# Optimization experiments

Measured on AMD Instinct MI355X. Metric: run time of the kernel, lower is better.

## Reference

```python
import jax, jax.numpy as jnp
import numpy as np


def setup_inputs() -> dict:
    key = jax.random.key(0)
    k1, k2, k3, k4 = jax.random.split(key, 4)
    n, C, t, h, w = 1, 256, 8, 64, 64
    heads = 8
    S = t + h + w - 2  # 134 axial positions per query
    attention = jax.random.normal(k1, (n, heads * S, t, h, w), dtype=jnp.float32)
    value = jax.random.normal(k2, (n, C, t, h, w), dtype=jnp.float32)
    conv_w = jax.random.normal(k3, (C, C), dtype=jnp.float32) / np.float32(np.sqrt(C))
    conv_b = jax.random.normal(k4, (C,), dtype=jnp.float32)
    return {"attention": attention, "value": value, "conv_w": conv_w,
            "conv_b": conv_b, "num_heads": heads}


def _grid_attn_map(A, V):
    """Criss-cross axial attention aggregation.
    A: [b, t+h+w-2, t, h, w] per-query weights over the t-axis (t entries,
       self included), h-axis (h-1 entries, self excluded) and w-axis
       (w-1 entries, self excluded).
    V: [b, c, t, h, w]. Returns [b, c, t, h, w].
    """
    b, c, t, h, w = V.shape
    A_t = A[:, :t]                  # [b, t, t, h, w]
    A_h = A[:, t:t + h - 1]         # [b, h-1, t, h, w]
    A_w = A[:, t + h - 1:]          # [b, w-1, t, h, w]

    # t-axis (self included): sum over key frame s
    out = jnp.einsum('bsthw,bcshw->bcthw', A_t, V)

    # h-axis (self excluded): channel j addresses key row p = j + (j >= q).
    # Build dense [h] channel axis with a zero at p == q via a padded gather.
    zpad = jnp.zeros((b, 1, t, h, w), A.dtype)
    A_h_pad = jnp.concatenate([A_h, zpad], axis=1)  # channel h-1 is zero
    p = jnp.arange(h)[:, None]
    q = jnp.arange(h)[None, :]
    inv_h = jnp.where(p < q, p, jnp.where(p == q, h - 1, p - 1))  # [h(p), h(q)]
    A_h_full = jnp.take_along_axis(A_h_pad, inv_h[None, :, None, :, None], axis=1)  # [b,p,t,q,w]
    out = out + jnp.einsum('bptqw,bctpw->bctqw', A_h_full, V)

    # w-axis (self excluded), same trick along w
    A_w_pad = jnp.concatenate([A_w, zpad], axis=1)  # channel w-1 is zero (h==w here OK; recompute pad generally)
    pw = jnp.arange(w)[:, None]
    qw = jnp.arange(w)[None, :]
    inv_w = jnp.where(pw < qw, pw, jnp.where(pw == qw, w - 1, pw - 1))  # [w(p), w(q)]
    A_w_full = jnp.take_along_axis(A_w_pad, inv_w[None, :, None, None, :], axis=1)  # [b,p,t,h,q]
    out = out + jnp.einsum('bpthq,bcthp->bcthq', A_w_full, V)
    return out


def reference(attention, value, conv_w, conv_b, num_heads):
    n, C, t, h, w = value.shape
    S = t + h + w - 2
    # 1x1x1 Conv3d == per-position channel matmul
    pv = jnp.einsum('ncthw,oc->nothw', value, conv_w) + conv_b[None, :, None, None, None]
    pv = pv.reshape(n * num_heads, C // num_heads, t, h, w)
    A = attention.reshape(n * num_heads, S, t, h, w)
    out = _grid_attn_map(A, pv)
    return out.reshape(n, num_heads, C // num_heads, t, h, w)
```

## Files before the change

### kernel.cpp

```cpp
#include <hip/hip_runtime.h>

#define SS   134
#define HWP  4096
#define THW  32768

typedef float f32x4 __attribute__((ext_vector_type(4)));
typedef short bf16x8 __attribute__((ext_vector_type(8)));
typedef short bf16x4 __attribute__((ext_vector_type(4)));

__device__ __forceinline__ unsigned short f2bf(float f) {
  unsigned int u = __float_as_uint(f);
  u += 0x7fff + ((u >> 16) & 1);
  return (unsigned short)(u >> 16);
}

__global__ __launch_bounds__(256) void conv1x1_v2(
    const float* __restrict__ V, const float* __restrict__ W,
    const float* __restrict__ bias, float* __restrict__ PV) {
  __shared__ unsigned short sW[256 * 40];
  __shared__ unsigned short sV[32 * 40];
  const int tid = threadIdx.x;
  const int x0 = blockIdx.x * 32;
  const int lane = tid & 63;
  const int wv = tid >> 6;
  const int m = lane & 15;
  const int q = lane >> 4;

  f32x4 acc[4][2];
#pragma unroll
  for (int i = 0; i < 4; ++i)
#pragma unroll
    for (int j = 0; j < 2; ++j)
      acc[i][j] = (f32x4){0.f, 0.f, 0.f, 0.f};

  for (int k0 = 0; k0 < 256; k0 += 32) {
#pragma unroll 2
    for (int r = 0; r < 8; ++r) {
      const int f = r * 256 + tid;
      const int o = f >> 3;
      const int c4 = (f & 7) * 4;
      const float4 w4 = *(const float4*)&W[o * 256 + k0 + c4];
      bf16x4 b;
      b.x = (short)f2bf(w4.x);
      b.y = (short)f2bf(w4.y);
      b.z = (short)f2bf(w4.z);
      b.w = (short)f2bf(w4.w);
      *(bf16x4*)&sW[o * 40 + c4] = b;
    }
    {
      const int c = tid >> 3;
      const int x4 = (tid & 7) * 4;
      const float4 v4 = *(const float4*)&V[(size_t)(k0 + c) * THW + x0 + x4];
      sV[(x4 + 0) * 40 + c] = f2bf(v4.x);
      sV[(x4 + 1) * 40 + c] = f2bf(v4.y);
      sV[(x4 + 2) * 40 + c] = f2bf(v4.z);
      sV[(x4 + 3) * 40 + c] = f2bf(v4.w);
    }
    __syncthreads();
    bf16x8 fa[4], fb[2];
#pragma unroll
    for (int i = 0; i < 4; ++i)
      fa[i] = *(const bf16x8*)&sW[(wv * 64 + i * 16 + m) * 40 + q * 8];
#pragma unroll
    for (int j = 0; j < 2; ++j)
      fb[j] = *(const bf16x8*)&sV[(j * 16 + m) * 40 + q * 8];
#pragma unroll
    for (int i = 0; i < 4; ++i)
#pragma unroll
      for (int j = 0; j < 2; ++j)
        acc[i][j] = __builtin_amdgcn_mfma_f32_16x16x32_bf16(fa[i], fb[j], acc[i][j], 0, 0, 0);
    __syncthreads();
  }

#pragma unroll
  for (int i = 0; i < 4; ++i) {
#pragma unroll
    for (int r = 0; r < 4; ++r) {
      const int o = wv * 64 + i * 16 + q * 4 + r;
      const float b = bias[o];
#pragma unroll
      for (int j = 0; j < 2; ++j)
        PV[(size_t)o * THW + x0 + j * 16 + m] = acc[i][j][r] + b;
    }
  }
}

__global__ __launch_bounds__(256) void attn_th(
    const float* __restrict__ A, const float* __restrict__ PV,
    float* __restrict__ O) {
  const int b = blockIdx.x;
  const int wb = b & 7;
  const int tq = (b >> 3) & 7;
  const int hd = b >> 6;
  const int tid = threadIdx.x;
  const int w4 = (tid & 1) * 4;
  const int q16 = (tid >> 1) & 15;
  const int cg = tid >> 5;

  __shared__ float slab[32 * 64 * 8];

  const float* __restrict__ Ab = A + (size_t)hd * SS * THW + (size_t)tq * HWP;
  const size_t pvh = (size_t)hd * 32 * THW;

#pragma unroll 4
  for (int i = 0; i < 16; ++i) {
    const int fid = tid + i * 256;
    const int ws = (fid & 1) * 4;
    const int p = (fid >> 1) & 63;
    const int c = fid >> 7;
    *(f32x4*)&slab[(c * 64 + p) * 8 + ws] =
        *(const f32x4*)&PV[pvh + (size_t)c * THW + (size_t)tq * HWP + p * 64 + wb * 8 + ws];
  }
  __syncthreads();

  f32x4 acc[4][4];
#pragma unroll
  for (int i = 0; i < 4; ++i)
#pragma unroll
    for (int j = 0; j < 4; ++j)
      acc[i][j] = (f32x4){0.f, 0.f, 0.f, 0.f};

  for (int s = 0; s < 8; ++s) {
#pragma unroll
    for (int qq = 0; qq < 4; ++qq) {
      const int q = qq * 16 + q16;
      const f32x4 a = *(const f32x4*)&Ab[(size_t)s * THW + q * 64 + wb * 8 + w4];
#pragma unroll
      for (int ci = 0; ci < 4; ++ci) {
        const int c = cg + ci * 8;
        const f32x4 v =
            *(const f32x4*)&PV[pvh + (size_t)c * THW + (size_t)s * HWP + q * 64 + wb * 8 + w4];
        acc[qq][ci] += a * v;
      }
    }
  }

  const float* __restrict__ Ah = Ab + (size_t)8 * THW + wb * 8 + w4;
#pragma unroll 2
  for (int p = 0; p < 64; ++p) {
    f32x4 av[4];
#pragma unroll
    for (int qq = 0; qq < 4; ++qq) {
      const int q = qq * 16 + q16;
      const int row = p - (q < p ? 1 : 0);
      f32x4 a = *(const f32x4*)&Ah[(size_t)row * THW + q * 64];
      if (q == p) a = (f32x4){0.f, 0.f, 0.f, 0.f};
      av[qq] = a;
    }
    f32x4 vv[4];
#pragma unroll
    for (int ci = 0; ci < 4; ++ci)
      vv[ci] = *(const f32x4*)&slab[((cg + ci * 8) * 64 + p) * 8 + w4];
#pragma unroll
    for (int qq = 0; qq < 4; ++qq)
#pragma unroll
      for (int ci = 0; ci < 4; ++ci)
        acc[qq][ci] += av[qq] * vv[ci];
  }

#pragma unroll
  for (int qq = 0; qq < 4; ++qq) {
    const int q = qq * 16 + q16;
#pragma unroll
    for (int ci = 0; ci < 4; ++ci) {
      const int c = cg + ci * 8;
      *(f32x4*)&O[pvh + (size_t)c * THW + (size_t)tq * HWP + q * 64 + wb * 8 + w4] =
          acc[qq][ci];
    }
  }
}

__global__ __launch_bounds__(256) void attn_w(
    const float* __restrict__ A, const float* __restrict__ PV,
    float* __restrict__ O) {
  const int b = blockIdx.x;
  const int hb = b & 15;
  const int tq = (b >> 4) & 7;
  const int hd = b >> 7;
  const int tid = threadIdx.x;
  const int wq = tid & 63;
  const int cg = tid >> 6;
  const int h0 = hb * 4;

  __shared__ float slab[32 * 64 * 4];

  const float* __restrict__ Ab = A + (size_t)hd * SS * THW + (size_t)tq * HWP;
  const size_t pvh = (size_t)hd * 32 * THW;

#pragma unroll 4
  for (int i = 0; i < 8; ++i) {
    const int fid = tid + i * 256;
    const int w4s = (fid & 15) * 4;
    const int h = (fid >> 4) & 3;
    const int c = fid >> 6;
    const f32x4 v =
        *(const f32x4*)&PV[pvh + (size_t)c * THW + (size_t)tq * HWP + (h0 + h) * 64 + w4s];
    slab[(c * 64 + w4s + 0) * 4 + h] = v.x;
    slab[(c * 64 + w4s + 1) * 4 + h] = v.y;
    slab[(c * 64 + w4s + 2) * 4 + h] = v.z;
    slab[(c * 64 + w4s + 3) * 4 + h] = v.w;
  }

  f32x4 racc[8];
#pragma unroll
  for (int ci = 0; ci < 8; ++ci) {
    const int c = cg + ci * 4;
    f32x4 r;
#pragma unroll
    for (int hh = 0; hh < 4; ++hh)
      r[hh] = O[pvh + (size_t)c * THW + (size_t)tq * HWP + (h0 + hh) * 64 + wq];
    racc[ci] = r;
  }
  __syncthreads();

#pragma unroll 2
  for (int p = 0; p < 64; ++p) {
    const int row = 71 + p - (wq <= p ? 1 : 0);
    const float* pa = Ab + (size_t)row * THW + h0 * 64 + wq;
    f32x4 a;
    a.x = pa[0];
    a.y = pa[64];
    a.z = pa[128];
    a.w = pa[192];
    if (p == wq) a = (f32x4){0.f, 0.f, 0.f, 0.f};
#pragma unroll
    for (int ci = 0; ci < 8; ++ci) {
      const f32x4 v = *(const f32x4*)&slab[(cg + ci * 4) * 256 + p * 4];
      racc[ci] += a * v;
    }
  }

#pragma unroll
  for (int ci = 0; ci < 8; ++ci) {
    const int c = cg + ci * 4;
#pragma unroll
    for (int hh = 0; hh < 4; ++hh)
      O[pvh + (size_t)c * THW + (size_t)tq * HWP + (h0 + hh) * 64 + wq] = racc[ci][hh];
  }
}

extern "C" void kernel_launch(void* const* d_in, const int* in_sizes, int n_in,
                              void* d_out, int out_size, void* d_ws, size_t ws_size,
                              hipStream_t stream) {
  const float* A = (const float*)d_in[0];
  const float* V = (const float*)d_in[1];
  const float* W = (const float*)d_in[2];
  const float* bias = (const float*)d_in[3];
  float* out = (float*)d_out;
  float* pv = (float*)d_ws;

  conv1x1_v2<<<dim3(1024), 256, 0, stream>>>(V, W, bias, pv);
  attn_th<<<dim3(512), 256, 0, stream>>>(A, pv, out);
  attn_w<<<dim3(1024), 256, 0, stream>>>(A, pv, out);
}
```

Baseline: 380.8 us.

## Retile attn_th over full w rows with double-buffered PV staging in shared memory

attn_th now uses 256 blocks of 512 threads. Each block covers one head, one frame and 16 query rows across the full 64-wide w axis, instead of an 8-wide w strip. The h-axis PV slab is streamed in chunks of 8 rows through a double-buffered 128KB shared buffer, with the next chunk's global loads prefetched into registers while the current chunk is computed. This gives each wave full 256-byte coalesced rows for the A and PV loads and keeps the large slab from limiting occupancy. The cost is fewer blocks (256), extra barriers per chunk, and 128KB of LDS per block, which allows only one block per CU.

```diff
diff --git a/kernel.cpp b/kernel.cpp
--- a/kernel.cpp
+++ b/kernel.cpp
@@ -85,33 +85,27 @@
   }
 }
 
-__global__ __launch_bounds__(256) void attn_th(
+__global__ __launch_bounds__(512) void attn_th(
     const float* __restrict__ A, const float* __restrict__ PV,
     float* __restrict__ O) {
   const int b = blockIdx.x;
-  const int wb = b & 7;
-  const int tq = (b >> 3) & 7;
-  const int hd = b >> 6;
+  const int hd = b & 7;
+  const int qb = (b >> 3) & 3;
+  const int tq = b >> 5;
   const int tid = threadIdx.x;
-  const int w4 = (tid & 1) * 4;
-  const int q16 = (tid >> 1) & 15;
-  const int cg = tid >> 5;
-
-  __shared__ float slab[32 * 64 * 8];
+  const int lane = tid & 63;
+  const int wv = tid >> 6;
+  const int w4 = (lane & 15) * 4;
+  const int cl = lane >> 4;
+  const int ch = wv & 1;
+  const int qg = wv >> 1;
+  const int q0 = qb * 16 + qg * 4;
+
+  __shared__ float slab[2][8 * 32 * 64];
 
   const float* __restrict__ Ab = A + (size_t)hd * SS * THW + (size_t)tq * HWP;
   const size_t pvh = (size_t)hd * 32 * THW;
-
-#pragma unroll 4
-  for (int i = 0; i < 16; ++i) {
-    const int fid = tid + i * 256;
-    const int ws = (fid & 1) * 4;
-    const int p = (fid >> 1) & 63;
-    const int c = fid >> 7;
-    *(f32x4*)&slab[(c * 64 + p) * 8 + ws] =
-        *(const f32x4*)&PV[pvh + (size_t)c * THW + (size_t)tq * HWP + p * 64 + wb * 8 + ws];
-  }
-  __syncthreads();
+  const float* __restrict__ PVh = PV + pvh;
 
   f32x4 acc[4][4];
 #pragma unroll
@@ -120,52 +114,82 @@
     for (int j = 0; j < 4; ++j)
       acc[i][j] = (f32x4){0.f, 0.f, 0.f, 0.f};
 
+  const int c_s = tid >> 4;
+  const int w4s = (tid & 15) * 4;
+  const float* __restrict__ pvstage =
+      PVh + (size_t)c_s * THW + (size_t)tq * HWP + w4s;
+  const int sbase = c_s * 64 + w4s;
+
+  f32x4 stg[8];
+#pragma unroll
+  for (int r = 0; r < 8; ++r) stg[r] = *(const f32x4*)&pvstage[r * 64];
+
   for (int s = 0; s < 8; ++s) {
 #pragma unroll
-    for (int qq = 0; qq < 4; ++qq) {
-      const int q = qq * 16 + q16;
-      const f32x4 a = *(const f32x4*)&Ab[(size_t)s * THW + q * 64 + wb * 8 + w4];
-#pragma unroll
-      for (int ci = 0; ci < 4; ++ci) {
-        const int c = cg + ci * 8;
+    for (int qi = 0; qi < 4; ++qi) {
+      const int q = q0 + qi;
+      const f32x4 a = *(const f32x4*)&Ab[(size_t)s * THW + q * 64 + w4];
+#pragma unroll
+      for (int g = 0; g < 4; ++g) {
+        const int c = ch * 16 + g * 4 + cl;
         const f32x4 v =
-            *(const f32x4*)&PV[pvh + (size_t)c * THW + (size_t)s * HWP + q * 64 + wb * 8 + w4];
-        acc[qq][ci] += a * v;
+            *(const f32x4*)&PVh[(size_t)c * THW + (size_t)s * HWP + q * 64 + w4];
+        acc[qi][g] += a * v;
       }
     }
   }
 
-  const float* __restrict__ Ah = Ab + (size_t)8 * THW + wb * 8 + w4;
-#pragma unroll 2
-  for (int p = 0; p < 64; ++p) {
-    f32x4 av[4];
-#pragma unroll
-    for (int qq = 0; qq < 4; ++qq) {
-      const int q = qq * 16 + q16;
-      const int row = p - (q < p ? 1 : 0);
-      f32x4 a = *(const f32x4*)&Ah[(size_t)row * THW + q * 64];
-      if (q == p) a = (f32x4){0.f, 0.f, 0.f, 0.f};
-      av[qq] = a;
-    }
-    f32x4 vv[4];
-#pragma unroll
-    for (int ci = 0; ci < 4; ++ci)
-      vv[ci] = *(const f32x4*)&slab[((cg + ci * 8) * 64 + p) * 8 + w4];
-#pragma unroll
-    for (int qq = 0; qq < 4; ++qq)
-#pragma unroll
-      for (int ci = 0; ci < 4; ++ci)
-        acc[qq][ci] += av[qq] * vv[ci];
-  }
-
-#pragma unroll
-  for (int qq = 0; qq < 4; ++qq) {
-    const int q = qq * 16 + q16;
-#pragma unroll
-    for (int ci = 0; ci < 4; ++ci) {
-      const int c = cg + ci * 8;
-      *(f32x4*)&O[pvh + (size_t)c * THW + (size_t)tq * HWP + q * 64 + wb * 8 + w4] =
-          acc[qq][ci];
+#pragma unroll
+  for (int r = 0; r < 8; ++r)
+    *(f32x4*)&slab[0][r * 2048 + sbase] = stg[r];
+  __syncthreads();
+
+  for (int ck = 0; ck < 8; ++ck) {
+    const int cur = ck & 1;
+    if (ck < 7) {
+#pragma unroll
+      for (int r = 0; r < 8; ++r)
+        stg[r] = *(const f32x4*)&pvstage[((ck + 1) * 8 + r) * 64];
+    }
+#pragma unroll
+    for (int pp = 0; pp < 8; ++pp) {
+      const int p = ck * 8 + pp;
+      f32x4 a[4];
+#pragma unroll
+      for (int qi = 0; qi < 4; ++qi) {
+        const int q = q0 + qi;
+        const int row = p - (q < p ? 1 : 0);
+        f32x4 av = *(const f32x4*)&Ab[(size_t)(8 + row) * THW + q * 64 + w4];
+        if (q == p) av = (f32x4){0.f, 0.f, 0.f, 0.f};
+        a[qi] = av;
+      }
+      f32x4 v[4];
+#pragma unroll
+      for (int g = 0; g < 4; ++g)
+        v[g] = *(const f32x4*)&slab[cur][pp * 2048 + (ch * 16 + g * 4 + cl) * 64 + w4];
+#pragma unroll
+      for (int qi = 0; qi < 4; ++qi)
+#pragma unroll
+        for (int g = 0; g < 4; ++g)
+          acc[qi][g] += a[qi] * v[g];
+    }
+    __syncthreads();
+    if (ck < 7) {
+#pragma unroll
+      for (int r = 0; r < 8; ++r)
+        *(f32x4*)&slab[cur ^ 1][r * 2048 + sbase] = stg[r];
+      __syncthreads();
+    }
+  }
+
+#pragma unroll
+  for (int qi = 0; qi < 4; ++qi) {
+    const int q = q0 + qi;
+#pragma unroll
+    for (int g = 0; g < 4; ++g) {
+      const int c = ch * 16 + g * 4 + cl;
+      *(f32x4*)&O[pvh + (size_t)c * THW + (size_t)tq * HWP + q * 64 + w4] =
+          acc[qi][g];
     }
   }
 }
@@ -250,6 +274,6 @@
   float* pv = (float*)d_ws;
 
   conv1x1_v2<<<dim3(1024), 256, 0, stream>>>(V, W, bias, pv);
-  attn_th<<<dim3(512), 256, 0, stream>>>(A, pv, out);
+  attn_th<<<dim3(256), 512, 0, stream>>>(A, pv, out);
   attn_w<<<dim3(1024), 256, 0, stream>>>(A, pv, out);
 }
```

Result: faster. 347.7 us (-8.7%).
